# Optimization experiments

Measured on AMD Instinct MI355X. Metric: run time of the kernel, lower is better.

Reference implementation:

```python
import jax, jax.numpy as jnp
import numpy as np

N = 16384   # nodes (atoms)
E = 262144  # edges (avg degree 16)
C = 64      # hidden channels per degree
H = 8       # attention heads
L = 4       # layers
R = 32      # radial MLP hidden
AED = 32    # atom embedding dim
TED = 32    # timestep embedding dim
NT = 1000   # num diffusion timesteps
NA = 16     # num atom types
DIN = AED + TED


def _sinusoidal(seq_len, dim):
    pos = np.arange(seq_len, dtype=np.float32)[:, None]
    dims = np.arange(dim, dtype=np.float32)[None, :]
    ang = pos / 10000.0 ** (2.0 * np.floor(dims / 2.0) / dim)
    emb = np.zeros((seq_len, dim), dtype=np.float32)
    emb[:, 0::2] = np.sin(ang[:, 0::2])
    emb[:, 1::2] = np.cos(ang[:, 1::2])
    return jnp.asarray(emb)


def setup_inputs() -> dict:
    key = jax.random.key(0)
    ks = jax.random.split(key, 20)
    def w(k, shape, fan_in):
        return jax.random.normal(k, shape, jnp.float32) / np.float32(np.sqrt(fan_in))
    return {
        'coordinates': jax.random.normal(ks[0], (N, 3), jnp.float32),
        'embed_table': w(ks[1], (NA, AED), 1.0),
        't_emb': _sinusoidal(NT, TED),
        'Win_s': w(ks[2], (DIN, C), DIN),
        'Win_v': w(ks[3], (1, C), 1.0),
        'Wq_s': w(ks[4], (L, C, C), C),
        'Wq_v': w(ks[5], (L, C, C), C),
        'Wk_s': w(ks[6], (L, C, C), C),
        'Wk_v': w(ks[7], (L, C, C), C),
        'R_W1': w(ks[8], (L, 1, R), 1.0),
        'R_b1': jnp.zeros((L, R), jnp.float32),
        'R_W2': w(ks[9], (L, R, H * 8), R),
        'R_b2': jnp.zeros((L, H * 8), jnp.float32),
        'Wo_s': w(ks[10], (L, C, C), C),
        'Wo_v': w(ks[11], (L, C, C), C),
        'Wout_v': w(ks[12], (C, 1), C),
        'atoms': jax.random.randint(ks[13], (N,), 0, NA),
        'src': jax.random.randint(ks[14], (E,), 0, N),
        'dst': jax.random.randint(ks[15], (E,), 0, N),
        't': 500,
    }


def _forward(coordinates, embed_table, t_emb, Win_s, Win_v, Wq_s, Wq_v, Wk_s, Wk_v,
             R_W1, R_b1, R_W2, R_b2, Wo_s, Wo_v, Wout_v, atoms, src, dst, t):
    n = coordinates.shape[0]
    Ch = C // H
    # center coordinates (as in wrapper)
    x = coordinates - coordinates.mean(axis=0, keepdims=True)
    # degree-0 input: atom embedding ++ timestep embedding
    s = jnp.concatenate([embed_table[atoms], jnp.broadcast_to(t_emb[t], (n, TED))], axis=-1)
    s = s @ Win_s                                        # [N, C] scalars
    # degree-1 input: coordinates (1 channel), lifted to C channels
    v = jnp.einsum('nkd,kc->ncd', x[:, None, :], Win_v)  # [N, C, 3] vectors
    # edge geometry (spherical-harmonic basis up to l=1: Y0=const, Y1 ~ rhat)
    rel = x[dst] - x[src]
    d = jnp.sqrt(jnp.sum(rel * rel, axis=-1) + 1e-12)    # [E]
    rhat = rel / d[:, None]                              # [E, 3]
    rh = rhat[:, None, None, :]                          # [E,1,1,3]
    for l in range(L):
        # radial network -> per-head CG-path weights (key/value x {0->0,1->0,1->1,0->1})
        rad = (jax.nn.relu(d[:, None] @ R_W1[l] + R_b1[l]) @ R_W2[l] + R_b2[l]).reshape(-1, H, 8)
        k_s = (s @ Wk_s[l])[src].reshape(-1, H, Ch)                          # [E,H,Ch]
        k_v = jnp.einsum('ecd,cf->efd', v[src], Wk_v[l]).reshape(-1, H, Ch, 3)
        vdotr = jnp.einsum('ehcd,ed->ehc', k_v, rhat)                        # 1x1 -> 0 path
        key_s = rad[..., 0:1] * k_s + rad[..., 1:2] * vdotr
        key_v = rad[..., 2:3, None] * k_v + rad[..., 3:4, None] * k_s[..., None] * rh
        val_s = rad[..., 4:5] * k_s + rad[..., 5:6] * vdotr
        val_v = rad[..., 6:7, None] * k_v + rad[..., 7:8, None] * k_s[..., None] * rh
        q_s = (s @ Wq_s[l]).reshape(n, H, Ch)[dst]
        q_v = jnp.einsum('ncd,cf->nfd', v, Wq_v[l]).reshape(n, H, Ch, 3)[dst]
        # invariant attention logits over incoming edges
        logit = ((q_s * key_s).sum(-1) + (q_v * key_v).sum((-1, -2))) / np.float32(np.sqrt(Ch))
        m = jax.lax.stop_gradient(jax.ops.segment_max(logit, dst, num_segments=n))
        a = jnp.exp(logit - m[dst])
        denom = jax.ops.segment_sum(a, dst, num_segments=n)
        alpha = a / (denom[dst] + 1e-9)                                      # [E,H]
        agg_s = jax.ops.segment_sum(alpha[..., None] * val_s, dst, num_segments=n).reshape(n, C)
        agg_v = jax.ops.segment_sum(alpha[..., None, None] * val_v, dst, num_segments=n).reshape(n, C, 3)
        # self-interaction + residual + equivariant nonlinearity
        s = jax.nn.silu(s + agg_s @ Wo_s[l])
        vr = v + jnp.einsum('ncd,cf->nfd', agg_v, Wo_v[l])
        v = vr * jax.nn.sigmoid(jnp.sum(vr * vr, axis=-1, keepdims=True))    # norm gate
    # fiber_out degree-1 with 1 channel -> updated coordinates
    return jnp.einsum('ncd,ck->nkd', v, Wout_v)[:, 0, :]                     # [N, 3]


def reference(coordinates, embed_table, t_emb, Win_s, Win_v, Wq_s, Wq_v, Wk_s, Wk_v,
              R_W1, R_b1, R_W2, R_b2, Wo_s, Wo_v, Wout_v, atoms, src, dst, t):
    return _forward(coordinates, embed_table, t_emb, Win_s, Win_v, Wq_s, Wq_v, Wk_s, Wk_v,
                    R_W1, R_b1, R_W2, R_b2, Wo_s, Wo_v, Wout_v, atoms, src, dst, t)
```

## Files before the change

### kernel.cpp

```cpp
#include <hip/hip_runtime.h>
#include <math.h>

#define NN 16384
#define NE 262144

constexpr size_t OFF_PART  = 0;
constexpr size_t OFF_MEAN  = 256;
constexpr size_t OFF_T     = 512;
constexpr size_t OFF_BIAS  = 1536;
constexpr size_t OFF_S     = 2048;
constexpr size_t OFF_V     = OFF_S     + (size_t)NN * 64;
constexpr size_t OFF_GEOM  = OFF_V     + (size_t)NN * 192;
constexpr size_t OFF_GEOMC = OFF_GEOM  + (size_t)NE * 4;
constexpr size_t OFF_QS    = OFF_GEOMC + (size_t)NE * 4;
constexpr size_t OFF_KS    = OFF_QS    + (size_t)NN * 64;
constexpr size_t OFF_QV    = OFF_KS    + (size_t)NN * 64;
constexpr size_t OFF_KV    = OFF_QV    + (size_t)NN * 192;
constexpr size_t OFF_RAD   = OFF_KV    + (size_t)NN * 192;
constexpr size_t OFF_INT   = OFF_RAD   + (size_t)NE * 64;
constexpr size_t I_ROWPTR  = OFF_INT;
constexpr size_t I_CURSOR  = OFF_INT + 16640;
constexpr size_t I_SRCC    = I_CURSOR + (size_t)NN;

static __device__ __forceinline__ double sigmoidd_(double x) {
  return 1.0 / (1.0 + exp(-x));
}

static __device__ __forceinline__ double fast_exp(double x) {
  x = fmax(x, -708.0);
  double y = x * 1.4426950408889634074;
  double k = rint(y);
  double r = fma(k, -6.93147180369123816490e-01, x);
  r = fma(k, -1.90821492927058770002e-10, r);
  double p = 2.755731922398589e-7;
  p = fma(p, r, 2.7557319223985893e-6);
  p = fma(p, r, 2.48015873015873016e-5);
  p = fma(p, r, 1.98412698412698413e-4);
  p = fma(p, r, 1.38888888888888889e-3);
  p = fma(p, r, 8.33333333333333333e-3);
  p = fma(p, r, 4.16666666666666667e-2);
  p = fma(p, r, 1.66666666666666667e-1);
  p = fma(p, r, 0.5);
  p = fma(p, r, 1.0);
  p = fma(p, r, 1.0);
  long long ki = (long long)k;
  double sc = __longlong_as_double((unsigned long long)(1023LL + ki) << 52);
  return p * sc;
}

__global__ void k_mean_partial(const float* __restrict__ coords, float* __restrict__ partials) {
  __shared__ double sm[3][256];
  int tid = threadIdx.x;
  int n = blockIdx.x * 256 + tid;
  sm[0][tid] = (double)coords[n * 3 + 0];
  sm[1][tid] = (double)coords[n * 3 + 1];
  sm[2][tid] = (double)coords[n * 3 + 2];
  __syncthreads();
  for (int off = 128; off > 0; off >>= 1) {
    if (tid < off) {
      sm[0][tid] += sm[0][tid + off];
      sm[1][tid] += sm[1][tid + off];
      sm[2][tid] += sm[2][tid + off];
    }
    __syncthreads();
  }
  if (tid == 0) {
    partials[blockIdx.x * 3 + 0] = (float)sm[0][0];
    partials[blockIdx.x * 3 + 1] = (float)sm[1][0];
    partials[blockIdx.x * 3 + 2] = (float)sm[2][0];
  }
}

__global__ void k_mean_final(const float* __restrict__ partials, float* __restrict__ mean) {
  int lane = threadIdx.x;
  double s0 = (double)partials[lane * 3 + 0];
  double s1 = (double)partials[lane * 3 + 1];
  double s2 = (double)partials[lane * 3 + 2];
  for (int off = 32; off > 0; off >>= 1) {
    s0 += __shfl_xor(s0, off);
    s1 += __shfl_xor(s1, off);
    s2 += __shfl_xor(s2, off);
  }
  if (lane == 0) {
    mean[0] = (float)(s0 * (1.0 / (double)NN));
    mean[1] = (float)(s1 * (1.0 / (double)NN));
    mean[2] = (float)(s2 * (1.0 / (double)NN));
  }
}

__global__ void k_prep_T(const float* __restrict__ embed, const float* __restrict__ t_emb,
                         const float* __restrict__ Win_s, const int* __restrict__ tptr,
                         float* __restrict__ T, float* __restrict__ bias) {
  int f = threadIdx.x;
  int tv = tptr[0];
  double b = 0.0;
  for (int k = 0; k < 32; ++k)
    b = fma((double)t_emb[tv * 32 + k], (double)Win_s[(32 + k) * 64 + f], b);
  bias[f] = (float)b;
  for (int a = 0; a < 16; ++a) {
    double acc = 0.0;
    for (int k = 0; k < 32; ++k)
      acc = fma((double)embed[a * 32 + k], (double)Win_s[k * 64 + f], acc);
    T[a * 64 + f] = (float)acc;
  }
}

__global__ void k_init_nodes(const float* __restrict__ coords, const float* __restrict__ mean,
                             const int* __restrict__ atoms, const float* __restrict__ T,
                             const float* __restrict__ bias, const float* __restrict__ Win_v,
                             float* __restrict__ S, float* __restrict__ V) {
  int id = blockIdx.x * 256 + threadIdx.x;
  int n = id >> 6, c = id & 63;
  double x0 = (double)coords[n * 3 + 0] - (double)mean[0];
  double x1 = (double)coords[n * 3 + 1] - (double)mean[1];
  double x2 = (double)coords[n * 3 + 2] - (double)mean[2];
  int a = atoms[n];
  S[n * 64 + c] = T[a * 64 + c] + bias[c];
  double w = (double)Win_v[c];
  V[(n * 64 + c) * 3 + 0] = (float)(x0 * w);
  V[(n * 64 + c) * 3 + 1] = (float)(x1 * w);
  V[(n * 64 + c) * 3 + 2] = (float)(x2 * w);
}

__global__ void k_edge_geom(const float* __restrict__ coords, const int* __restrict__ src,
                            const int* __restrict__ dst, float4* __restrict__ geom,
                            int* __restrict__ count) {
  int e = blockIdx.x * 256 + threadIdx.x;
  int se = src[e], de = dst[e];
  double rx = (double)coords[de * 3 + 0] - (double)coords[se * 3 + 0];
  double ry = (double)coords[de * 3 + 1] - (double)coords[se * 3 + 1];
  double rz = (double)coords[de * 3 + 2] - (double)coords[se * 3 + 2];
  double d2 = rx * rx + ry * ry + rz * rz + 1e-12;
  double dd = sqrt(d2);
  double inv = 1.0 / dd;
  geom[e] = make_float4((float)dd, (float)(rx * inv), (float)(ry * inv), (float)(rz * inv));
  atomicAdd(&count[de], 1);
}

__global__ void k_scan(int* count_cursor, int* rowptr) {
  __shared__ int buf[256];
  __shared__ int carry_s;
  int tid = threadIdx.x;
  if (tid == 0) carry_s = 0;
  __syncthreads();
  for (int base = 0; base < NN; base += 256) {
    int idx = base + tid;
    int val = count_cursor[idx];
    buf[tid] = val;
    __syncthreads();
    int incl = val;
    for (int off = 1; off < 256; off <<= 1) {
      int t = (tid >= off) ? buf[tid - off] : 0;
      __syncthreads();
      incl += t;
      buf[tid] = incl;
      __syncthreads();
    }
    int excl = carry_s + incl - val;
    rowptr[idx] = excl;
    count_cursor[idx] = excl;
    __syncthreads();
    if (tid == 255) carry_s += incl;
    __syncthreads();
  }
  if (tid == 0) rowptr[NN] = carry_s;
}

__global__ void k_scatter(const int* __restrict__ dst, const int* __restrict__ src,
                          const float4* __restrict__ geom, int* __restrict__ cursor,
                          int* __restrict__ srcc, float4* __restrict__ geomc) {
  int e = blockIdx.x * 256 + threadIdx.x;
  int de = dst[e];
  int pos = atomicAdd(&cursor[de], 1);
  srcc[pos] = src[e];
  geomc[pos] = geom[e];
}

__global__ void k_rad(const float4* __restrict__ geomc,
                      const float* __restrict__ R_W1, const float* __restrict__ R_b1,
                      const float* __restrict__ R_W2, const float* __restrict__ R_b2,
                      float* __restrict__ radc, int l) {
  __shared__ float2 w1b1[32];
  __shared__ float b2s[64];
  __shared__ float w2s[2048];
  for (int i = threadIdx.x; i < 2048; i += 256) w2s[i] = R_W2[l * 2048 + i];
  if (threadIdx.x < 64) b2s[threadIdx.x] = R_b2[l * 64 + threadIdx.x];
  if (threadIdx.x < 32)
    w1b1[threadIdx.x] = make_float2(R_W1[l * 32 + threadIdx.x], R_b1[l * 32 + threadIdx.x]);
  __syncthreads();
  int lane = threadIdx.x & 63;
  float w2col[32];
#pragma unroll
  for (int r = 0; r < 32; ++r) w2col[r] = w2s[r * 64 + lane];
  double b2v = (double)b2s[lane];
  float2 hwb = w1b1[lane & 31];
  for (int j = blockIdx.x * 4 + (threadIdx.x >> 6); j < NE; j += 4096) {
    float dd = geomc[j].x;
    double hd = fma((double)dd, (double)hwb.x, (double)hwb.y);
    float hidf = (float)fmax(hd, 0.0);
    double rad = b2v;
#pragma unroll
    for (int r = 0; r < 32; ++r)
      rad = fma((double)__shfl(hidf, r), (double)w2col[r], rad);
    radc[((size_t)j << 6) + lane] = (float)rad;
  }
}

__global__ void k_node_s(const float* __restrict__ S,
                         const float* __restrict__ Wq_s, const float* __restrict__ Wk_s,
                         float* __restrict__ QS, float* __restrict__ KS, int l) {
  __shared__ float wqs[4096], wks[4096];
  for (int i = threadIdx.x; i < 4096; i += 512) {
    wqs[i] = Wq_s[l * 4096 + i];
    wks[i] = Wk_s[l * 4096 + i];
  }
  __syncthreads();
  int lane = threadIdx.x & 63;
  for (int n = blockIdx.x * 8 + (threadIdx.x >> 6); n < NN; n += 8192) {
    float sv = S[n * 64 + lane];
    double aqs = 0.0, aks = 0.0;
#pragma unroll 8
    for (int c = 0; c < 64; ++c) {
      double sc = (double)__shfl(sv, c);
      aqs = fma(sc, (double)wqs[c * 64 + lane], aqs);
      aks = fma(sc, (double)wks[c * 64 + lane], aks);
    }
    QS[n * 64 + lane] = (float)aqs;
    KS[n * 64 + lane] = (float)aks;
  }
}

__global__ void k_node_v(const float* __restrict__ V,
                         const float* __restrict__ Wq_v, const float* __restrict__ Wk_v,
                         float* __restrict__ QV, float* __restrict__ KV, int l) {
  __shared__ float wqv[4096], wkv[4096];
  for (int i = threadIdx.x; i < 4096; i += 512) {
    wqv[i] = Wq_v[l * 4096 + i];
    wkv[i] = Wk_v[l * 4096 + i];
  }
  __syncthreads();
  int lane = threadIdx.x & 63;
  for (int n = blockIdx.x * 8 + (threadIdx.x >> 6); n < NN; n += 8192) {
    float v0 = V[(n * 64 + lane) * 3 + 0];
    float v1 = V[(n * 64 + lane) * 3 + 1];
    float v2 = V[(n * 64 + lane) * 3 + 2];
    double aqv0 = 0.0, aqv1 = 0.0, aqv2 = 0.0;
    double akv0 = 0.0, akv1 = 0.0, akv2 = 0.0;
#pragma unroll 8
    for (int c = 0; c < 64; ++c) {
      double u0 = (double)__shfl(v0, c);
      double u1 = (double)__shfl(v1, c);
      double u2 = (double)__shfl(v2, c);
      double wq = (double)wqv[c * 64 + lane];
      double wk = (double)wkv[c * 64 + lane];
      aqv0 = fma(u0, wq, aqv0); aqv1 = fma(u1, wq, aqv1); aqv2 = fma(u2, wq, aqv2);
      akv0 = fma(u0, wk, akv0); akv1 = fma(u1, wk, akv1); akv2 = fma(u2, wk, akv2);
    }
    QV[(n * 64 + lane) * 3 + 0] = (float)aqv0;
    QV[(n * 64 + lane) * 3 + 1] = (float)aqv1;
    QV[(n * 64 + lane) * 3 + 2] = (float)aqv2;
    KV[(n * 64 + lane) * 3 + 0] = (float)akv0;
    KV[(n * 64 + lane) * 3 + 1] = (float)akv1;
    KV[(n * 64 + lane) * 3 + 2] = (float)akv2;
  }
}

__global__ void k_aggregate(const float* __restrict__ QS, const float* __restrict__ KS,
                            const float* __restrict__ QV, const float* __restrict__ KV,
                            const float4* __restrict__ geomc, const float* __restrict__ radc,
                            const int* __restrict__ rowptr, const int* __restrict__ srcc,
                            const float* __restrict__ Wo_s, const float* __restrict__ Wo_v,
                            float* __restrict__ S, float* __restrict__ V, int l) {
  __shared__ float wos[4096];
  __shared__ float wov[4096];
  for (int i = threadIdx.x; i < 4096; i += 512) {
    wos[i] = Wo_s[l * 4096 + i];
    wov[i] = Wo_v[l * 4096 + i];
  }
  __syncthreads();
  int lane = threadIdx.x & 63;
  int gb = lane & 56;
  for (int n = blockIdx.x * 8 + (threadIdx.x >> 6); n < NN; n += 8192) {
    double qs = (double)QS[n * 64 + lane];
    double qv0 = (double)QV[(n * 64 + lane) * 3 + 0];
    double qv1 = (double)QV[(n * 64 + lane) * 3 + 1];
    double qv2 = (double)QV[(n * 64 + lane) * 3 + 2];
    int rb = rowptr[n], re = rowptr[n + 1];
    double m = -INFINITY, denom = 0.0;
    double as_ = 0.0, av0 = 0.0, av1 = 0.0, av2 = 0.0;
    for (int j = rb; j < re; ++j) {
      int se = srcc[j];
      float4 g = geomc[j];
      const float4* rp = (const float4*)(radc + ((size_t)j << 6) + gb);
      float4 rA = rp[0];
      float4 rB = rp[1];
      double rh0 = (double)g.y, rh1 = (double)g.z, rh2 = (double)g.w;
      double ksv = (double)KS[se * 64 + lane];
      double kv0 = (double)KV[(se * 64 + lane) * 3 + 0];
      double kv1 = (double)KV[(se * 64 + lane) * 3 + 1];
      double kv2 = (double)KV[(se * 64 + lane) * 3 + 2];
      double c0 = (double)rA.x, c1 = (double)rA.y, c2 = (double)rA.z, c3 = (double)rA.w;
      double c4 = (double)rB.x, c5 = (double)rB.y, c6 = (double)rB.z, c7 = (double)rB.w;
      double vdr = kv0 * rh0 + kv1 * rh1 + kv2 * rh2;
      double keys = c0 * ksv + c1 * vdr;
      double vals = c4 * ksv + c5 * vdr;
      double kx = c3 * ksv;
      double vx = c7 * ksv;
      double keyv0 = fma(c2, kv0, kx * rh0);
      double keyv1 = fma(c2, kv1, kx * rh1);
      double keyv2 = fma(c2, kv2, kx * rh2);
      double valv0 = fma(c6, kv0, vx * rh0);
      double valv1 = fma(c6, kv1, vx * rh1);
      double valv2 = fma(c6, kv2, vx * rh2);
      double lg = qs * keys + qv0 * keyv0 + qv1 * keyv1 + qv2 * keyv2;
      lg += __shfl_xor(lg, 1);
      lg += __shfl_xor(lg, 2);
      lg += __shfl_xor(lg, 4);
      lg *= 0.35355339059327376220;
      double nm = fmax(m, lg);
      double sc = fast_exp(m - nm);
      double a = fast_exp(lg - nm);
      m = nm;
      denom = fma(denom, sc, a);
      as_ = fma(as_, sc, a * vals);
      av0 = fma(av0, sc, a * valv0);
      av1 = fma(av1, sc, a * valv1);
      av2 = fma(av2, sc, a * valv2);
    }
    double inv = 1.0 / (denom + 1e-9);
    float aggs = (float)(as_ * inv);
    float agv0 = (float)(av0 * inv), agv1 = (float)(av1 * inv), agv2 = (float)(av2 * inv);
    double os = 0.0, ov0 = 0.0, ov1 = 0.0, ov2 = 0.0;
#pragma unroll 8
    for (int c = 0; c < 64; ++c) {
      double asc = (double)__shfl(aggs, c);
      double b0 = (double)__shfl(agv0, c);
      double b1 = (double)__shfl(agv1, c);
      double b2 = (double)__shfl(agv2, c);
      os = fma(asc, (double)wos[c * 64 + lane], os);
      double w = (double)wov[c * 64 + lane];
      ov0 = fma(b0, w, ov0); ov1 = fma(b1, w, ov1); ov2 = fma(b2, w, ov2);
    }
    double sn = (double)S[n * 64 + lane] + os;
    sn = sn * sigmoidd_(sn);
    S[n * 64 + lane] = (float)sn;
    double vr0 = (double)V[(n * 64 + lane) * 3 + 0] + ov0;
    double vr1 = (double)V[(n * 64 + lane) * 3 + 1] + ov1;
    double vr2 = (double)V[(n * 64 + lane) * 3 + 2] + ov2;
    double nrm = vr0 * vr0 + vr1 * vr1 + vr2 * vr2;
    double sg = sigmoidd_(nrm);
    V[(n * 64 + lane) * 3 + 0] = (float)(vr0 * sg);
    V[(n * 64 + lane) * 3 + 1] = (float)(vr1 * sg);
    V[(n * 64 + lane) * 3 + 2] = (float)(vr2 * sg);
  }
}

__global__ void k_output(const float* __restrict__ V, const float* __restrict__ Wout,
                         float* __restrict__ out) {
  int lane = threadIdx.x & 63;
  int n = blockIdx.x * 4 + (threadIdx.x >> 6);
  double w = (double)Wout[lane];
  double p0 = (double)V[(n * 64 + lane) * 3 + 0] * w;
  double p1 = (double)V[(n * 64 + lane) * 3 + 1] * w;
  double p2 = (double)V[(n * 64 + lane) * 3 + 2] * w;
  for (int off = 32; off > 0; off >>= 1) {
    p0 += __shfl_xor(p0, off);
    p1 += __shfl_xor(p1, off);
    p2 += __shfl_xor(p2, off);
  }
  if (lane == 0) {
    out[n * 3 + 0] = (float)p0;
    out[n * 3 + 1] = (float)p1;
    out[n * 3 + 2] = (float)p2;
  }
}

extern "C" void kernel_launch(void* const* d_in, const int* in_sizes, int n_in,
                              void* d_out, int out_size, void* d_ws, size_t ws_size,
                              hipStream_t stream) {
  (void)in_sizes; (void)n_in; (void)out_size; (void)ws_size;
  const float* coords = (const float*)d_in[0];
  const float* embed  = (const float*)d_in[1];
  const float* t_emb  = (const float*)d_in[2];
  const float* Win_s  = (const float*)d_in[3];
  const float* Win_v  = (const float*)d_in[4];
  const float* Wq_s   = (const float*)d_in[5];
  const float* Wq_v   = (const float*)d_in[6];
  const float* Wk_s   = (const float*)d_in[7];
  const float* Wk_v   = (const float*)d_in[8];
  const float* R_W1   = (const float*)d_in[9];
  const float* R_b1   = (const float*)d_in[10];
  const float* R_W2   = (const float*)d_in[11];
  const float* R_b2   = (const float*)d_in[12];
  const float* Wo_s   = (const float*)d_in[13];
  const float* Wo_v   = (const float*)d_in[14];
  const float* Wout_v = (const float*)d_in[15];
  const int* atoms = (const int*)d_in[16];
  const int* src   = (const int*)d_in[17];
  const int* dst   = (const int*)d_in[18];
  const int* tptr  = (const int*)d_in[19];

  float* ws    = (float*)d_ws;
  float* part  = ws + OFF_PART;
  float* mean  = ws + OFF_MEAN;
  float* Tp    = ws + OFF_T;
  float* bias  = ws + OFF_BIAS;
  float* Sp    = ws + OFF_S;
  float* Vp    = ws + OFF_V;
  float4* geom  = (float4*)(ws + OFF_GEOM);
  float4* geomc = (float4*)(ws + OFF_GEOMC);
  float* QSp   = ws + OFF_QS;
  float* KSp   = ws + OFF_KS;
  float* QVp   = ws + OFF_QV;
  float* KVp   = ws + OFF_KV;
  float* radc  = ws + OFF_RAD;
  int* rowptr = (int*)d_ws + I_ROWPTR;
  int* cursor = (int*)d_ws + I_CURSOR;
  int* srcc   = (int*)d_ws + I_SRCC;

  k_mean_partial<<<64, 256, 0, stream>>>(coords, part);
  k_mean_final<<<1, 64, 0, stream>>>(part, mean);
  k_prep_T<<<1, 64, 0, stream>>>(embed, t_emb, Win_s, tptr, Tp, bias);
  k_init_nodes<<<4096, 256, 0, stream>>>(coords, mean, atoms, Tp, bias, Win_v, Sp, Vp);

  hipMemsetAsync(cursor, 0, NN * sizeof(int), stream);
  k_edge_geom<<<NE / 256, 256, 0, stream>>>(coords, src, dst, geom, cursor);
  k_scan<<<1, 256, 0, stream>>>(cursor, rowptr);
  k_scatter<<<NE / 256, 256, 0, stream>>>(dst, src, geom, cursor, srcc, geomc);

  for (int l = 0; l < 4; ++l) {
    k_rad<<<1024, 256, 0, stream>>>(geomc, R_W1, R_b1, R_W2, R_b2, radc, l);
    k_node_s<<<1024, 512, 0, stream>>>(Sp, Wq_s, Wk_s, QSp, KSp, l);
    k_node_v<<<1024, 512, 0, stream>>>(Vp, Wq_v, Wk_v, QVp, KVp, l);
    k_aggregate<<<1024, 512, 0, stream>>>(QSp, KSp, QVp, KVp, geomc, radc, rowptr, srcc,
                                          Wo_s, Wo_v, Sp, Vp, l);
  }

  k_output<<<4096, 256, 0, stream>>>(Vp, Wout_v, (float*)d_out);
}
```

Before: 1.319 ms.

## Parallelize CSR scan and fuse per-layer radial/node projections into one launch

Replaces the single-block serial prefix scan over node degrees with a three-kernel multi-block scan (block scans, block-sum scan, add offsets). Merges the radial MLP, scalar Q/K projection and vector Q/K projection into one heterogeneous kernel whose blocks are partitioned by role, cutting launches per layer and letting independent work overlap on the GPU. This trades separate tuned grids for a fixed block split (512/384/128), which may unbalance the workload across roles.

New measurement: 1.228 ms. 1.07x faster.

```diff
diff --git a/kernel.cpp b/kernel.cpp
--- a/kernel.cpp
+++ b/kernel.cpp
@@ -137,33 +137,43 @@
   atomicAdd(&count[de], 1);
 }
 
-__global__ void k_scan(int* count_cursor, int* rowptr) {
+__global__ void k_scan1(const int* __restrict__ count, int* __restrict__ rowptr,
+                        int* __restrict__ bsum) {
   __shared__ int buf[256];
-  __shared__ int carry_s;
-  int tid = threadIdx.x;
-  if (tid == 0) carry_s = 0;
+  int tid = threadIdx.x, idx = blockIdx.x * 256 + tid;
+  int val = count[idx];
+  buf[tid] = val;
   __syncthreads();
-  for (int base = 0; base < NN; base += 256) {
-    int idx = base + tid;
-    int val = count_cursor[idx];
-    buf[tid] = val;
-    __syncthreads();
-    int incl = val;
-    for (int off = 1; off < 256; off <<= 1) {
-      int t = (tid >= off) ? buf[tid - off] : 0;
-      __syncthreads();
-      incl += t;
-      buf[tid] = incl;
-      __syncthreads();
-    }
-    int excl = carry_s + incl - val;
-    rowptr[idx] = excl;
-    count_cursor[idx] = excl;
-    __syncthreads();
-    if (tid == 255) carry_s += incl;
-    __syncthreads();
-  }
-  if (tid == 0) rowptr[NN] = carry_s;
+  int incl = val;
+  for (int off = 1; off < 256; off <<= 1) {
+    int t = (tid >= off) ? buf[tid - off] : 0;
+    __syncthreads();
+    incl += t;
+    buf[tid] = incl;
+    __syncthreads();
+  }
+  rowptr[idx] = incl - val;
+  if (tid == 255) bsum[blockIdx.x] = incl;
+}
+
+__global__ void k_scan2(int* __restrict__ bsum, int* __restrict__ rowptr) {
+  int lane = threadIdx.x;
+  int v = bsum[lane];
+  int incl = v;
+  for (int off = 1; off < 64; off <<= 1) {
+    int t = __shfl_up(incl, off);
+    if (lane >= off) incl += t;
+  }
+  bsum[lane] = incl - v;
+  if (lane == 63) rowptr[NN] = incl;
+}
+
+__global__ void k_scan3(int* __restrict__ rowptr, int* __restrict__ cursor,
+                        const int* __restrict__ bsum) {
+  int idx = blockIdx.x * 256 + threadIdx.x;
+  int v = rowptr[idx] + bsum[blockIdx.x];
+  rowptr[idx] = v;
+  cursor[idx] = v;
 }
 
 __global__ void k_scatter(const int* __restrict__ dst, const int* __restrict__ src,
@@ -176,92 +186,100 @@
   geomc[pos] = geom[e];
 }
 
-__global__ void k_rad(const float4* __restrict__ geomc,
-                      const float* __restrict__ R_W1, const float* __restrict__ R_b1,
-                      const float* __restrict__ R_W2, const float* __restrict__ R_b2,
-                      float* __restrict__ radc, int l) {
-  __shared__ float2 w1b1[32];
-  __shared__ float b2s[64];
-  __shared__ float w2s[2048];
-  for (int i = threadIdx.x; i < 2048; i += 256) w2s[i] = R_W2[l * 2048 + i];
-  if (threadIdx.x < 64) b2s[threadIdx.x] = R_b2[l * 64 + threadIdx.x];
-  if (threadIdx.x < 32)
-    w1b1[threadIdx.x] = make_float2(R_W1[l * 32 + threadIdx.x], R_b1[l * 32 + threadIdx.x]);
-  __syncthreads();
+#define RAD_B 512
+#define NV_B  384
+__global__ __launch_bounds__(512) void k_layer_pre(
+    const float4* __restrict__ geomc,
+    const float* __restrict__ R_W1, const float* __restrict__ R_b1,
+    const float* __restrict__ R_W2, const float* __restrict__ R_b2,
+    float* __restrict__ radc,
+    const float* __restrict__ S,
+    const float* __restrict__ Wq_s, const float* __restrict__ Wk_s,
+    float* __restrict__ QS, float* __restrict__ KS,
+    const float* __restrict__ V,
+    const float* __restrict__ Wq_v, const float* __restrict__ Wk_v,
+    float* __restrict__ QV, float* __restrict__ KV, int l) {
+  __shared__ float smem[8192];
   int lane = threadIdx.x & 63;
-  float w2col[32];
+  int wv = threadIdx.x >> 6;
+  if (blockIdx.x < RAD_B) {
+    float* w2s = smem;
+    float* b2s = smem + 2048;
+    float2* w1b1 = (float2*)(smem + 2112);
+    for (int i = threadIdx.x; i < 2048; i += 512) w2s[i] = R_W2[l * 2048 + i];
+    if (threadIdx.x < 64) b2s[threadIdx.x] = R_b2[l * 64 + threadIdx.x];
+    if (threadIdx.x < 32)
+      w1b1[threadIdx.x] = make_float2(R_W1[l * 32 + threadIdx.x], R_b1[l * 32 + threadIdx.x]);
+    __syncthreads();
+    double w2d[32];
 #pragma unroll
-  for (int r = 0; r < 32; ++r) w2col[r] = w2s[r * 64 + lane];
-  double b2v = (double)b2s[lane];
-  float2 hwb = w1b1[lane & 31];
-  for (int j = blockIdx.x * 4 + (threadIdx.x >> 6); j < NE; j += 4096) {
-    float dd = geomc[j].x;
-    double hd = fma((double)dd, (double)hwb.x, (double)hwb.y);
-    float hidf = (float)fmax(hd, 0.0);
-    double rad = b2v;
+    for (int r = 0; r < 32; ++r) w2d[r] = (double)w2s[r * 64 + lane];
+    double b2v = (double)b2s[lane];
+    float2 hwb = w1b1[lane & 31];
+    int j0 = blockIdx.x * 8 + wv;
+    for (int j = j0; j < NE; j += 4096) {
+      float dd = geomc[j].x;
+      double hd = fma((double)dd, (double)hwb.x, (double)hwb.y);
+      float hidf = (float)fmax(hd, 0.0);
+      double rad = b2v;
 #pragma unroll
-    for (int r = 0; r < 32; ++r)
-      rad = fma((double)__shfl(hidf, r), (double)w2col[r], rad);
-    radc[((size_t)j << 6) + lane] = (float)rad;
-  }
-}
-
-__global__ void k_node_s(const float* __restrict__ S,
-                         const float* __restrict__ Wq_s, const float* __restrict__ Wk_s,
-                         float* __restrict__ QS, float* __restrict__ KS, int l) {
-  __shared__ float wqs[4096], wks[4096];
-  for (int i = threadIdx.x; i < 4096; i += 512) {
-    wqs[i] = Wq_s[l * 4096 + i];
-    wks[i] = Wk_s[l * 4096 + i];
-  }
-  __syncthreads();
-  int lane = threadIdx.x & 63;
-  for (int n = blockIdx.x * 8 + (threadIdx.x >> 6); n < NN; n += 8192) {
-    float sv = S[n * 64 + lane];
-    double aqs = 0.0, aks = 0.0;
+      for (int r = 0; r < 32; ++r)
+        rad = fma((double)__shfl(hidf, r), w2d[r], rad);
+      radc[((size_t)j << 6) + lane] = (float)rad;
+    }
+  } else if (blockIdx.x < RAD_B + NV_B) {
+    float* wqv = smem;
+    float* wkv = smem + 4096;
+    for (int i = threadIdx.x; i < 4096; i += 512) {
+      wqv[i] = Wq_v[l * 4096 + i];
+      wkv[i] = Wk_v[l * 4096 + i];
+    }
+    __syncthreads();
+    int slot = (blockIdx.x - RAD_B) * 8 + wv;
+    for (int n = slot; n < NN; n += 3072) {
+      float v0 = V[(n * 64 + lane) * 3 + 0];
+      float v1 = V[(n * 64 + lane) * 3 + 1];
+      float v2 = V[(n * 64 + lane) * 3 + 2];
+      double aqv0 = 0.0, aqv1 = 0.0, aqv2 = 0.0;
+      double akv0 = 0.0, akv1 = 0.0, akv2 = 0.0;
 #pragma unroll 8
-    for (int c = 0; c < 64; ++c) {
-      double sc = (double)__shfl(sv, c);
-      aqs = fma(sc, (double)wqs[c * 64 + lane], aqs);
-      aks = fma(sc, (double)wks[c * 64 + lane], aks);
-    }
-    QS[n * 64 + lane] = (float)aqs;
-    KS[n * 64 + lane] = (float)aks;
-  }
-}
-
-__global__ void k_node_v(const float* __restrict__ V,
-                         const float* __restrict__ Wq_v, const float* __restrict__ Wk_v,
-                         float* __restrict__ QV, float* __restrict__ KV, int l) {
-  __shared__ float wqv[4096], wkv[4096];
-  for (int i = threadIdx.x; i < 4096; i += 512) {
-    wqv[i] = Wq_v[l * 4096 + i];
-    wkv[i] = Wk_v[l * 4096 + i];
-  }
-  __syncthreads();
-  int lane = threadIdx.x & 63;
-  for (int n = blockIdx.x * 8 + (threadIdx.x >> 6); n < NN; n += 8192) {
-    float v0 = V[(n * 64 + lane) * 3 + 0];
-    float v1 = V[(n * 64 + lane) * 3 + 1];
-    float v2 = V[(n * 64 + lane) * 3 + 2];
-    double aqv0 = 0.0, aqv1 = 0.0, aqv2 = 0.0;
-    double akv0 = 0.0, akv1 = 0.0, akv2 = 0.0;
+      for (int c = 0; c < 64; ++c) {
+        double u0 = (double)__shfl(v0, c);
+        double u1 = (double)__shfl(v1, c);
+        double u2 = (double)__shfl(v2, c);
+        double wq = (double)wqv[c * 64 + lane];
+        double wk = (double)wkv[c * 64 + lane];
+        aqv0 = fma(u0, wq, aqv0); aqv1 = fma(u1, wq, aqv1); aqv2 = fma(u2, wq, aqv2);
+        akv0 = fma(u0, wk, akv0); akv1 = fma(u1, wk, akv1); akv2 = fma(u2, wk, akv2);
+      }
+      QV[(n * 64 + lane) * 3 + 0] = (float)aqv0;
+      QV[(n * 64 + lane) * 3 + 1] = (float)aqv1;
+      QV[(n * 64 + lane) * 3 + 2] = (float)aqv2;
+      KV[(n * 64 + lane) * 3 + 0] = (float)akv0;
+      KV[(n * 64 + lane) * 3 + 1] = (float)akv1;
+      KV[(n * 64 + lane) * 3 + 2] = (float)akv2;
+    }
+  } else {
+    float* wqs = smem;
+    float* wks = smem + 4096;
+    for (int i = threadIdx.x; i < 4096; i += 512) {
+      wqs[i] = Wq_s[l * 4096 + i];
+      wks[i] = Wk_s[l * 4096 + i];
+    }
+    __syncthreads();
+    int slot = (blockIdx.x - RAD_B - NV_B) * 8 + wv;
+    for (int n = slot; n < NN; n += 1024) {
+      float sv = S[n * 64 + lane];
+      double aqs = 0.0, aks = 0.0;
 #pragma unroll 8
-    for (int c = 0; c < 64; ++c) {
-      double u0 = (double)__shfl(v0, c);
-      double u1 = (double)__shfl(v1, c);
-      double u2 = (double)__shfl(v2, c);
-      double wq = (double)wqv[c * 64 + lane];
-      double wk = (double)wkv[c * 64 + lane];
-      aqv0 = fma(u0, wq, aqv0); aqv1 = fma(u1, wq, aqv1); aqv2 = fma(u2, wq, aqv2);
-      akv0 = fma(u0, wk, akv0); akv1 = fma(u1, wk, akv1); akv2 = fma(u2, wk, akv2);
-    }
-    QV[(n * 64 + lane) * 3 + 0] = (float)aqv0;
-    QV[(n * 64 + lane) * 3 + 1] = (float)aqv1;
-    QV[(n * 64 + lane) * 3 + 2] = (float)aqv2;
-    KV[(n * 64 + lane) * 3 + 0] = (float)akv0;
-    KV[(n * 64 + lane) * 3 + 1] = (float)akv1;
-    KV[(n * 64 + lane) * 3 + 2] = (float)akv2;
+      for (int c = 0; c < 64; ++c) {
+        double sc = (double)__shfl(sv, c);
+        aqs = fma(sc, (double)wqs[c * 64 + lane], aqs);
+        aks = fma(sc, (double)wks[c * 64 + lane], aks);
+      }
+      QS[n * 64 + lane] = (float)aqs;
+      KS[n * 64 + lane] = (float)aks;
+    }
   }
 }
 
@@ -414,6 +432,7 @@
   float* QVp   = ws + OFF_QV;
   float* KVp   = ws + OFF_KV;
   float* radc  = ws + OFF_RAD;
+  int* bsum   = (int*)d_ws + OFF_PART;
   int* rowptr = (int*)d_ws + I_ROWPTR;
   int* cursor = (int*)d_ws + I_CURSOR;
   int* srcc   = (int*)d_ws + I_SRCC;
@@ -425,13 +444,15 @@
 
   hipMemsetAsync(cursor, 0, NN * sizeof(int), stream);
   k_edge_geom<<<NE / 256, 256, 0, stream>>>(coords, src, dst, geom, cursor);
-  k_scan<<<1, 256, 0, stream>>>(cursor, rowptr);
+  k_scan1<<<64, 256, 0, stream>>>(cursor, rowptr, bsum);
+  k_scan2<<<1, 64, 0, stream>>>(bsum, rowptr);
+  k_scan3<<<64, 256, 0, stream>>>(rowptr, cursor, bsum);
   k_scatter<<<NE / 256, 256, 0, stream>>>(dst, src, geom, cursor, srcc, geomc);
 
   for (int l = 0; l < 4; ++l) {
-    k_rad<<<1024, 256, 0, stream>>>(geomc, R_W1, R_b1, R_W2, R_b2, radc, l);
-    k_node_s<<<1024, 512, 0, stream>>>(Sp, Wq_s, Wk_s, QSp, KSp, l);
-    k_node_v<<<1024, 512, 0, stream>>>(Vp, Wq_v, Wk_v, QVp, KVp, l);
+    k_layer_pre<<<1024, 512, 0, stream>>>(geomc, R_W1, R_b1, R_W2, R_b2, radc,
+                                          Sp, Wq_s, Wk_s, QSp, KSp,
+                                          Vp, Wq_v, Wk_v, QVp, KVp, l);
     k_aggregate<<<1024, 512, 0, stream>>>(QSp, KSp, QVp, KVp, geomc, radc, rowptr, srcc,
                                           Wo_s, Wo_v, Sp, Vp, l);
   }
```
